# Optimization experiments

Measured on AMD Instinct MI355X. Metric: run time of the kernel, lower is better.

Reference implementation:

```python
import jax, jax.numpy as jnp
import numpy as np

TOP_K = 13
NUM_CLASSES = 80
ALPHA = 1.0
BETA = 6.0
EPS = 1e-9
IOU_EPS = 1e-7


def _ciou(box1, box2, eps=IOU_EPS):
    # box1: gt [B,M,1,4], box2: pred [B,1,A,4], corner format x1y1x2y2
    b1x1, b1y1, b1x2, b1y2 = jnp.split(box1, 4, axis=-1)
    b2x1, b2y1, b2x2, b2y2 = jnp.split(box2, 4, axis=-1)
    w1, h1 = b1x2 - b1x1, b1y2 - b1y1 + eps
    w2, h2 = b2x2 - b2x1, b2y2 - b2y1 + eps
    inter = (jnp.clip(jnp.minimum(b1x2, b2x2) - jnp.maximum(b1x1, b2x1), 0, None)
             * jnp.clip(jnp.minimum(b1y2, b2y2) - jnp.maximum(b1y1, b2y1), 0, None))
    union = w1 * h1 + w2 * h2 - inter + eps
    iou = inter / union
    cw = jnp.maximum(b1x2, b2x2) - jnp.minimum(b1x1, b2x1)  # enclosing box
    ch = jnp.maximum(b1y2, b2y2) - jnp.minimum(b1y1, b2y1)
    c2 = cw ** 2 + ch ** 2 + eps
    rho2 = ((b2x1 + b2x2 - b1x1 - b1x2) ** 2 + (b2y1 + b2y2 - b1y1 - b1y2) ** 2) / 4.0
    v = (4.0 / np.pi ** 2) * (jnp.arctan(w2 / h2) - jnp.arctan(w1 / h1)) ** 2
    alpha = v / (v - iou + (1.0 + eps))
    return (iou - (rho2 / c2 + v * alpha))[..., 0]  # [B,M,A]


def _assign(pred_cls, pred_bbox, anchor_points, gt_cls, gt_bbox, mask_gt):
    B, A, C = pred_cls.shape
    M = gt_bbox.shape[1]
    # --- anchors inside gt boxes: [B,M,A] ---
    lt, rb = gt_bbox[:, :, None, :2], gt_bbox[:, :, None, 2:]   # [B,M,1,2]
    xy = anchor_points[None, None]                               # [1,1,A,2]
    deltas = jnp.concatenate([xy - lt, rb - xy], axis=-1)        # [B,M,A,4]
    mask_in_gts = (deltas.min(-1) > EPS).astype(pred_bbox.dtype)
    mask = mask_in_gts * mask_gt                                 # mask_gt [B,M,1] broadcasts
    # --- box metrics: gather class scores at gt labels, full CIoU grid masked ---
    labels = gt_cls[..., 0].astype(jnp.int32)                    # [B,M]
    idx = jnp.broadcast_to(labels[:, None, :], (B, A, M))
    bbox_scores = jnp.take_along_axis(pred_cls, idx, axis=2).transpose(0, 2, 1) * mask
    overlaps = jnp.clip(_ciou(gt_bbox[:, :, None], pred_bbox[:, None]), 0, None) * mask
    align_metric = bbox_scores ** ALPHA * overlaps ** BETA       # [B,M,A]
    # --- top-k candidate selection (indices of masked-out gts forced to 0, dup counts zeroed) ---
    _, topk_idx = jax.lax.top_k(align_metric, TOP_K)             # [B,M,K]
    topk_mask = jnp.broadcast_to(mask_gt > 0, (B, M, TOP_K))
    topk_idx = jnp.where(topk_mask, topk_idx, 0)
    bi = jnp.arange(B)[:, None, None]
    mi = jnp.arange(M)[None, :, None]
    count = jnp.zeros((B, M, A), jnp.int32).at[bi, mi, topk_idx].add(1)
    mask_topk = jnp.where(count > 1, 0, count).astype(align_metric.dtype)
    mask_pos = mask_topk * mask_in_gts * mask_gt                 # [B,M,A]
    # --- resolve anchors claimed by multiple gts via max overlap ---
    fg = mask_pos.sum(-2)                                        # [B,A]
    is_max = jax.nn.one_hot(overlaps.argmax(1), M, dtype=mask_pos.dtype).transpose(0, 2, 1)
    mask_pos = jnp.where(fg[:, None, :] > 1, is_max, mask_pos)
    fg_mask = mask_pos.sum(-2)                                   # [B,A]
    target_gt_idx = mask_pos.argmax(-2)                          # [B,A]
    # --- gather targets ---
    flat = target_gt_idx + jnp.arange(B)[:, None] * M
    target_labels = labels.reshape(-1)[flat]                     # [B,A]
    target_bbox = gt_bbox.reshape(-1, 4)[flat]                   # [B,A,4]
    target_cls = jnp.where(fg_mask[..., None] > 0,
                           jax.nn.one_hot(target_labels, C, dtype=pred_cls.dtype), 0.0)
    # --- normalize scores by aligned metric ---
    align_metric = align_metric * mask_pos
    pos_align = align_metric.max(-1, keepdims=True)              # [B,M,1]
    pos_overlap = (overlaps * mask_pos).max(-1, keepdims=True)   # [B,M,1]
    norm = (align_metric * pos_overlap / (pos_align + EPS)).max(-2)[..., None]  # [B,A,1]
    target_cls = target_cls * norm
    return target_cls, target_bbox, fg_mask


def setup_inputs() -> dict:
    key = jax.random.key(0)
    ks = jax.random.split(key, 8)
    B, A, C, M = 16, 8400, 80, 32
    anchor_points = jax.random.uniform(ks[0], (A, 2)) * 80.0
    pred_cls = jax.random.uniform(ks[1], (B, A, C))  # sigmoid-like scores in [0,1)
    ctr = anchor_points[None] + jax.random.normal(ks[2], (B, A, 2)) * 2.0
    sz = jax.random.uniform(ks[3], (B, A, 2)) * 15.0 + 2.0
    pred_bbox = jnp.concatenate([ctr - sz / 2, ctr + sz / 2], axis=-1)
    gctr = jax.random.uniform(ks[4], (B, M, 2)) * 80.0
    gsz = jax.random.uniform(ks[5], (B, M, 2)) * 25.0 + 3.0
    gt_bbox = jnp.concatenate([gctr - gsz / 2, gctr + gsz / 2], axis=-1)
    gt_cls = jax.random.randint(ks[6], (B, M, 1), 0, C).astype(jnp.int64)
    mask_gt = (jax.random.uniform(ks[7], (B, M, 1)) < 0.8).astype(jnp.float32)
    return {"pred_cls": pred_cls, "pred_bbox": pred_bbox, "anchor_points": anchor_points,
            "gt_cls": gt_cls, "gt_bbox": gt_bbox, "mask_gt": mask_gt}


def reference(pred_cls, pred_bbox, anchor_points, gt_cls, gt_bbox, mask_gt):
    target_cls, target_bbox, fg_mask = _assign(pred_cls, pred_bbox, anchor_points,
                                               gt_cls, gt_bbox, mask_gt)
    return target_cls, target_bbox, fg_mask.astype(bool)
```

## Files before the change

kernel.cpp:

```cpp
#include <hip/hip_runtime.h>
#include <cstdint>
#include <cstddef>

#define BB 16
#define AA 8400
#define CC 80
#define MM 32
#define TOPK 13
#define NW 8
#define CANCH 1056

__device__ __forceinline__ float ciou_clip(
    float gx1, float gy1, float gx2, float gy2, float at1,
    float4 pb, float w2, float h2, float at2)
{
  const float w1 = gx2 - gx1, h1 = gy2 - gy1 + 1e-7f;
  const float iw = fmaxf(fminf(gx2, pb.z) - fmaxf(gx1, pb.x), 0.f);
  const float ih = fmaxf(fminf(gy2, pb.w) - fmaxf(gy1, pb.y), 0.f);
  const float inter = iw * ih;
  const float uni = w1*h1 + w2*h2 - inter + 1e-7f;
  const float iou = inter / uni;
  const float cw = fmaxf(gx2, pb.z) - fminf(gx1, pb.x);
  const float ch = fmaxf(gy2, pb.w) - fminf(gy1, pb.y);
  const float c2 = cw*cw + ch*ch + 1e-7f;
  const float rx = pb.x + pb.z - gx1 - gx2;
  const float ry = pb.y + pb.w - gy1 - gy2;
  const float rho2 = (rx*rx + ry*ry) * 0.25f;
  const float dv = at2 - at1;
  const float v = 0.4052847345693511f * dv * dv;
  const float alpha = v / (v - iou + (1.f + 1e-7f));
  return fmaxf(iou - (rho2 / c2 + v * alpha), 0.f);
}

__device__ __forceinline__ unsigned long long pack_key(float val, int a) {
  return ((unsigned long long)__float_as_uint(val) << 32)
       | (unsigned long long)(0xFFFFFFFFu - (unsigned)a);
}
__device__ __forceinline__ int key_anchor(unsigned long long k) {
  return (int)(0xFFFFFFFFu - (unsigned)(k & 0xFFFFFFFFull));
}

__global__ __launch_bounds__(512) void k_topk(
    const float* __restrict__ pred_cls, const float* __restrict__ pred_bbox,
    const float* __restrict__ anchors, const int* __restrict__ gt_cls,
    const float* __restrict__ gt_bbox, const float* __restrict__ mask_gt,
    unsigned long long* __restrict__ topkeys)
{
  const int m = blockIdx.x, b = blockIdx.y;
  const int tid = threadIdx.x;
  const int wave = tid >> 6, lane = tid & 63;

  unsigned long long* tk = topkeys + (size_t)(b*MM + m)*TOPK;
  if (mask_gt[b*MM + m] <= 0.f) {
    if (tid < TOPK) tk[tid] = 0ull;
    return;
  }

  __shared__ unsigned short q[NW][CANCH];
  __shared__ unsigned long long s_top[NW][TOPK];

  const float4 gb = reinterpret_cast<const float4*>(gt_bbox)[b*MM + m];
  const float at1 = atanf((gb.z - gb.x) / (gb.w - gb.y + 1e-7f));
  const int lbl = gt_cls[b*MM + m];
  const float*  clsbase = pred_cls + (size_t)b*AA*CC;
  const float4* pbase   = reinterpret_cast<const float4*>(pred_bbox) + (size_t)b*AA;
  const float2* axy     = reinterpret_cast<const float2*>(anchors);

  unsigned long long k13[TOPK];
  #pragma unroll
  for (int i = 0; i < TOPK; ++i) k13[i] = 0ull;

  if (wave == 0) {
    const int a = lane;
    const float2 xy = axy[a];
    const float mind = fminf(fminf(xy.x - gb.x, xy.y - gb.y),
                             fminf(gb.z - xy.x, gb.w - xy.y));
    float val = 0.f;
    if (mind > 1e-9f) {
      const float4 pb = pbase[a];
      const float w2 = pb.z - pb.x, h2 = pb.w - pb.y + 1e-7f;
      const float at2 = atanf(w2 / h2);
      const float ov = ciou_clip(gb.x, gb.y, gb.z, gb.w, at1, pb, w2, h2, at2);
      const float o2 = ov * ov;
      val = clsbase[(size_t)a*CC + lbl] * (o2 * o2 * o2);
    }
    k13[0] = pack_key(val, a);
  }

  const int abase = wave * CANCH;
  int qc = 0;
  for (int s = 0; s < 17; ++s) {
    const int la = s*64 + lane;
    const int a  = abase + la;
    bool pass = false;
    if (la < CANCH && a < AA && !(wave == 0 && a < 64)) {
      const float2 xy = axy[a];
      const float mind = fminf(fminf(xy.x - gb.x, xy.y - gb.y),
                               fminf(gb.z - xy.x, gb.w - xy.y));
      pass = mind > 1e-9f;
    }
    const unsigned long long bal = __ballot(pass);
    if (pass) {
      const int pos = qc + (int)__popcll(bal & ((1ull << lane) - 1ull));
      q[wave][pos] = (unsigned short)la;
    }
    qc += (int)__popcll(bal);
  }

  for (int k = lane; k < qc; k += 64) {
    const int a = abase + (int)q[wave][k];
    const float4 pb = pbase[a];
    const float w2 = pb.z - pb.x, h2 = pb.w - pb.y + 1e-7f;
    const float at2 = atanf(w2 / h2);
    const float ov = ciou_clip(gb.x, gb.y, gb.z, gb.w, at1, pb, w2, h2, at2);
    const float o2 = ov * ov;
    const float val = clsbase[(size_t)a*CC + lbl] * (o2 * o2 * o2);
    const unsigned long long key = pack_key(val, a);
    if (key > k13[TOPK-1]) {
      #pragma unroll
      for (int i = TOPK-1; i >= 1; --i)
        if (key > k13[i]) k13[i] = (key > k13[i-1]) ? k13[i-1] : key;
      if (key > k13[0]) k13[0] = key;
    }
  }

  for (int r = 0; r < TOPK; ++r) {
    unsigned long long bk = k13[0];
    #pragma unroll
    for (int off = 32; off; off >>= 1) {
      const unsigned long long o = __shfl_xor(bk, off);
      if (o > bk) bk = o;
    }
    if (k13[0] == bk) {
      #pragma unroll
      for (int i = 0; i < TOPK-1; ++i) k13[i] = k13[i+1];
      k13[TOPK-1] = 0ull;
    }
    if (lane == 0) s_top[wave][r] = bk;
  }
  __syncthreads();
  if (wave != 0) return;

  unsigned long long v0 = 0ull, v1 = 0ull;
  {
    const int e0 = lane, e1 = lane + 64;
    v0 = s_top[e0/TOPK][e0%TOPK];
    if (e1 < NW*TOPK) v1 = s_top[e1/TOPK][e1%TOPK];
  }
  for (int r = 0; r < TOPK; ++r) {
    const bool s1 = v1 > v0;
    unsigned long long bk = s1 ? v1 : v0;
    const unsigned long long my = bk;
    #pragma unroll
    for (int off = 32; off; off >>= 1) {
      const unsigned long long o = __shfl_xor(bk, off);
      if (o > bk) bk = o;
    }
    if (lane == 0) tk[r] = bk;
    if (my == bk && bk != 0ull) {
      if (s1) v1 = 0ull; else v0 = 0ull;
    }
  }
}

__global__ __launch_bounds__(512) void k_assign(
    const float* __restrict__ pred_cls, const float* __restrict__ pred_bbox,
    const float* __restrict__ anchors, const int* __restrict__ gt_cls,
    const float* __restrict__ gt_bbox, const float* __restrict__ mask_gt,
    const unsigned long long* __restrict__ topkeys,
    float* __restrict__ out_cls, float* __restrict__ out_bbox,
    float* __restrict__ out_fg)
{
  const int b = blockIdx.x / 17, ch = blockIdx.x % 17;
  const int tid = threadIdx.x;
  const int lane = tid & 63;
  const int w0 = ch * 512;
  const int nw = (w0 + 512 <= AA) ? 512 : (AA - w0);

  __shared__ unsigned int s_claim[AA];
  __shared__ unsigned short s_list[MM*TOPK];
  __shared__ int s_ncl;
  __shared__ unsigned char s_asg[512];
  __shared__ float s_av[512];
  __shared__ unsigned int s_pal[MM], s_pov[MM];
  __shared__ float4 s_gb[MM];
  __shared__ float s_at[MM], s_mgt[MM];
  __shared__ int s_lbl[MM];

  const float2* axy   = reinterpret_cast<const float2*>(anchors);
  const float4* pbase = reinterpret_cast<const float4*>(pred_bbox) + (size_t)b*AA;

  if (tid < MM) {
    const float4 g = reinterpret_cast<const float4*>(gt_bbox)[b*MM + tid];
    s_gb[tid] = g;
    s_at[tid] = atanf((g.z - g.x) / (g.w - g.y + 1e-7f));
    s_lbl[tid] = gt_cls[b*MM + tid];
    s_mgt[tid] = mask_gt[b*MM + tid];
    s_pal[tid] = 0u; s_pov[tid] = 0u;
  }
  if (tid == 0) s_ncl = 0;
  s_asg[tid] = 255;
  for (int k = tid; k < AA; k += 512) s_claim[k] = 0u;
  __syncthreads();

  if (tid < MM*TOPK) {
    const int m = tid / TOPK;
    const unsigned long long key = topkeys[(size_t)(b*MM + m)*TOPK + tid%TOPK];
    const int a = key_anchor(key);
    if ((unsigned)a < (unsigned)AA) {
      const float2 xy = axy[a];
      const float4 g = s_gb[m];
      const float mind = fminf(fminf(xy.x - g.x, xy.y - g.y),
                               fminf(g.z - xy.x, g.w - xy.y));
      if (mind > 1e-9f) atomicOr(&s_claim[a], 1u << m);
    }
  }
  __syncthreads();

  for (int a = tid; a < AA; a += 512) {
    const bool c = s_claim[a] != 0u;
    const unsigned long long bal = __ballot(c);
    int base = 0;
    if (lane == 0 && bal) base = atomicAdd(&s_ncl, (int)__popcll(bal));
    base = __shfl(base, 0);
    if (c) s_list[base + (int)__popcll(bal & ((1ull << lane) - 1ull))]
             = (unsigned short)a;
  }
  __syncthreads();
  const int ncl = s_ncl;

  for (int k = tid; k < ncl; k += 512) {
    const int a = (int)s_list[k];
    const unsigned cb = s_claim[a];
    const float4 pb = pbase[a];
    const float2 xy = axy[a];
    const float w2 = pb.z - pb.x, h2 = pb.w - pb.y + 1e-7f;
    const float at2 = atanf(w2 / h2);
    int asg; float bestov;
    if (__popc(cb) == 1) {
      asg = __ffs(cb) - 1;
      const float4 g = s_gb[asg];
      bestov = ciou_clip(g.x, g.y, g.z, g.w, s_at[asg], pb, w2, h2, at2);
    } else {
      float best = -1.f; int bm = 0;
      for (int m = 0; m < MM; ++m) {
        float ov = 0.f;
        const float4 g = s_gb[m];
        const float mind = fminf(fminf(xy.x - g.x, xy.y - g.y),
                                 fminf(g.z - xy.x, g.w - xy.y));
        if (mind > 1e-9f && s_mgt[m] > 0.f)
          ov = ciou_clip(g.x, g.y, g.z, g.w, s_at[m], pb, w2, h2, at2);
        if (ov > best) { best = ov; bm = m; }
      }
      asg = bm; bestov = best;
    }
    const float o2 = bestov * bestov;
    const float av = pred_cls[(size_t)(b*AA + a)*CC + s_lbl[asg]] * (o2*o2*o2);
    atomicMax(&s_pal[asg], __float_as_uint(av));
    atomicMax(&s_pov[asg], __float_as_uint(bestov));
    const int wi = a - w0;
    if ((unsigned)wi < (unsigned)nw) { s_asg[wi] = (unsigned char)asg; s_av[wi] = av; }
  }
  __syncthreads();

  float4* ocw = reinterpret_cast<float4*>(out_cls) + ((size_t)(b*AA + w0)) * (CC/4);
  for (int j = tid; j < nw*(CC/4); j += 512) {
    const int ai = j / (CC/4);
    const int q4 = j % (CC/4);
    const int asg = s_asg[ai];
    float4 o = make_float4(0.f, 0.f, 0.f, 0.f);
    if (asg != 255) {
      const float norm = s_av[ai] * __uint_as_float(s_pov[asg])
                       / (__uint_as_float(s_pal[asg]) + 1e-9f);
      const int lbl = s_lbl[asg];
      const int c0 = q4 * 4;
      if (lbl == c0    ) o.x = norm;
      if (lbl == c0 + 1) o.y = norm;
      if (lbl == c0 + 2) o.z = norm;
      if (lbl == c0 + 3) o.w = norm;
    }
    ocw[j] = o;
  }
  if (tid < nw) {
    const int a = w0 + tid;
    const int asg = s_asg[tid];
    const int tgt = (asg != 255) ? asg : 0;
    reinterpret_cast<float4*>(out_bbox)[b*AA + a] = s_gb[tgt];
    out_fg[b*AA + a] = (asg != 255) ? 1.f : 0.f;
  }
}

extern "C" void kernel_launch(void* const* d_in, const int* in_sizes, int n_in,
                              void* d_out, int out_size, void* d_ws, size_t ws_size,
                              hipStream_t stream)
{
  const float* pred_cls  = (const float*)d_in[0];
  const float* pred_bbox = (const float*)d_in[1];
  const float* anchors   = (const float*)d_in[2];
  const int*   gt_cls    = (const int*)  d_in[3];
  const float* gt_bbox   = (const float*)d_in[4];
  const float* mask_gt   = (const float*)d_in[5];

  unsigned long long* topkeys = (unsigned long long*)d_ws;

  float* out_cls  = (float*)d_out;
  float* out_bbox = out_cls + (size_t)BB*AA*CC;
  float* out_fg   = out_bbox + (size_t)BB*AA*4;

  k_topk<<<dim3(MM, BB), 512, 0, stream>>>(
      pred_cls, pred_bbox, anchors, gt_cls, gt_bbox, mask_gt, topkeys);
  k_assign<<<dim3(BB*17), 512, 0, stream>>>(
      pred_cls, pred_bbox, anchors, gt_cls, gt_bbox, mask_gt, topkeys,
      out_cls, out_bbox, out_fg);
}
```

Before: 48.61 us.

## Split top-k anchor scan across two blocks per GT and merge in assign

Each GT's top-k search is split into two blocks that each cover half of the anchors and write a partial top-13 list. The assign kernel then loads both partial lists into shared memory and merge-selects the final 13 per GT. This doubles the top-k grid from 512 to 1024 blocks to improve GPU occupancy and shorten per-block work. In exchange it adds a serial merge step and a larger workspace for keys.

```diff
diff --git a/kernel.cpp b/kernel.cpp
--- a/kernel.cpp
+++ b/kernel.cpp
@@ -8,7 +8,8 @@
 #define MM 32
 #define TOPK 13
 #define NW 8
-#define CANCH 1056
+#define HANCH 4224
+#define CANCH 528
 
 __device__ __forceinline__ float ciou_clip(
     float gx1, float gy1, float gx2, float gy2, float at1,
@@ -46,11 +47,11 @@
     const float* __restrict__ gt_bbox, const float* __restrict__ mask_gt,
     unsigned long long* __restrict__ topkeys)
 {
-  const int m = blockIdx.x, b = blockIdx.y;
+  const int m = blockIdx.x >> 1, half = blockIdx.x & 1, b = blockIdx.y;
   const int tid = threadIdx.x;
   const int wave = tid >> 6, lane = tid & 63;
 
-  unsigned long long* tk = topkeys + (size_t)(b*MM + m)*TOPK;
+  unsigned long long* tk = topkeys + ((size_t)(b*MM + m)*2 + half)*TOPK;
   if (mask_gt[b*MM + m] <= 0.f) {
     if (tid < TOPK) tk[tid] = 0ull;
     return;
@@ -70,7 +71,7 @@
   #pragma unroll
   for (int i = 0; i < TOPK; ++i) k13[i] = 0ull;
 
-  if (wave == 0) {
+  if (half == 0 && wave == 0) {
     const int a = lane;
     const float2 xy = axy[a];
     const float mind = fminf(fminf(xy.x - gb.x, xy.y - gb.y),
@@ -87,13 +88,13 @@
     k13[0] = pack_key(val, a);
   }
 
-  const int abase = wave * CANCH;
+  const int abase = half*HANCH + wave*CANCH;
   int qc = 0;
-  for (int s = 0; s < 17; ++s) {
+  for (int s = 0; s < 9; ++s) {
     const int la = s*64 + lane;
     const int a  = abase + la;
     bool pass = false;
-    if (la < CANCH && a < AA && !(wave == 0 && a < 64)) {
+    if (la < CANCH && a < AA && !(half == 0 && wave == 0 && la < 64)) {
       const float2 xy = axy[a];
       const float mind = fminf(fminf(xy.x - gb.x, xy.y - gb.y),
                                fminf(gb.z - xy.x, gb.w - xy.y));
@@ -178,6 +179,8 @@
   const int nw = (w0 + 512 <= AA) ? 512 : (AA - w0);
 
   __shared__ unsigned int s_claim[AA];
+  __shared__ unsigned long long s_keys[MM*2*TOPK];
+  __shared__ int s_sel[MM][TOPK];
   __shared__ unsigned short s_list[MM*TOPK];
   __shared__ int s_ncl;
   __shared__ unsigned char s_asg[512];
@@ -200,13 +203,26 @@
   }
   if (tid == 0) s_ncl = 0;
   s_asg[tid] = 255;
+  for (int k = tid; k < MM*2*TOPK; k += 512)
+    s_keys[k] = topkeys[(size_t)b*MM*2*TOPK + k];
   for (int k = tid; k < AA; k += 512) s_claim[k] = 0u;
+  __syncthreads();
+
+  if (tid < MM) {
+    const unsigned long long* A = s_keys + (size_t)tid*2*TOPK;
+    const unsigned long long* B = A + TOPK;
+    int i = 0, j = 0;
+    for (int r = 0; r < TOPK; ++r) {
+      const unsigned long long ka = A[i], kb = B[j];
+      if (ka >= kb) { s_sel[tid][r] = key_anchor(ka); ++i; }
+      else          { s_sel[tid][r] = key_anchor(kb); ++j; }
+    }
+  }
   __syncthreads();
 
   if (tid < MM*TOPK) {
     const int m = tid / TOPK;
-    const unsigned long long key = topkeys[(size_t)(b*MM + m)*TOPK + tid%TOPK];
-    const int a = key_anchor(key);
+    const int a = s_sel[m][tid % TOPK];
     if ((unsigned)a < (unsigned)AA) {
       const float2 xy = axy[a];
       const float4 g = s_gb[m];
@@ -307,7 +323,7 @@
   float* out_bbox = out_cls + (size_t)BB*AA*CC;
   float* out_fg   = out_bbox + (size_t)BB*AA*4;
 
-  k_topk<<<dim3(MM, BB), 512, 0, stream>>>(
+  k_topk<<<dim3(MM*2, BB), 512, 0, stream>>>(
       pred_cls, pred_bbox, anchors, gt_cls, gt_bbox, mask_gt, topkeys);
   k_assign<<<dim3(BB*17), 512, 0, stream>>>(
       pred_cls, pred_bbox, anchors, gt_cls, gt_bbox, mask_gt, topkeys,
```

After: 60.50 us. +24.4%, slower.

## Split assignment into per-batch position kernel and wide output-writing kernel

Applied to the files above, without the earlier changes.

Before, each of the 17 chunk blocks per batch recomputed the full anchor assignment, then wrote only its own window. Now one block per batch computes the claim, assignment and per-gt max statistics once and stores them in workspace. A second kernel with many small 256-thread blocks reads that state back and writes the dense class, bbox and foreground outputs. This removes the redundant recomputation and spreads the large output writes over more blocks, at the cost of an extra launch, a global-memory round trip and only 16 blocks in the compute stage.

```diff
diff --git a/kernel.cpp b/kernel.cpp
--- a/kernel.cpp
+++ b/kernel.cpp
@@ -163,25 +163,21 @@
   }
 }
 
-__global__ __launch_bounds__(512) void k_assign(
+__global__ __launch_bounds__(512) void k_pos(
     const float* __restrict__ pred_cls, const float* __restrict__ pred_bbox,
     const float* __restrict__ anchors, const int* __restrict__ gt_cls,
     const float* __restrict__ gt_bbox, const float* __restrict__ mask_gt,
     const unsigned long long* __restrict__ topkeys,
-    float* __restrict__ out_cls, float* __restrict__ out_bbox,
-    float* __restrict__ out_fg)
-{
-  const int b = blockIdx.x / 17, ch = blockIdx.x % 17;
+    unsigned char* __restrict__ asg_arr, float* __restrict__ av_arr,
+    float* __restrict__ pos_align, float* __restrict__ pos_ovl)
+{
+  const int b = blockIdx.x;
   const int tid = threadIdx.x;
   const int lane = tid & 63;
-  const int w0 = ch * 512;
-  const int nw = (w0 + 512 <= AA) ? 512 : (AA - w0);
 
   __shared__ unsigned int s_claim[AA];
   __shared__ unsigned short s_list[MM*TOPK];
   __shared__ int s_ncl;
-  __shared__ unsigned char s_asg[512];
-  __shared__ float s_av[512];
   __shared__ unsigned int s_pal[MM], s_pov[MM];
   __shared__ float4 s_gb[MM];
   __shared__ float s_at[MM], s_mgt[MM];
@@ -199,8 +195,10 @@
     s_pal[tid] = 0u; s_pov[tid] = 0u;
   }
   if (tid == 0) s_ncl = 0;
-  s_asg[tid] = 255;
-  for (int k = tid; k < AA; k += 512) s_claim[k] = 0u;
+  for (int a = tid; a < AA; a += 512) {
+    s_claim[a] = 0u;
+    asg_arr[(size_t)b*AA + a] = 255;
+  }
   __syncthreads();
 
   if (tid < MM*TOPK) {
@@ -258,20 +256,57 @@
     const float av = pred_cls[(size_t)(b*AA + a)*CC + s_lbl[asg]] * (o2*o2*o2);
     atomicMax(&s_pal[asg], __float_as_uint(av));
     atomicMax(&s_pov[asg], __float_as_uint(bestov));
-    const int wi = a - w0;
-    if ((unsigned)wi < (unsigned)nw) { s_asg[wi] = (unsigned char)asg; s_av[wi] = av; }
-  }
-  __syncthreads();
-
-  float4* ocw = reinterpret_cast<float4*>(out_cls) + ((size_t)(b*AA + w0)) * (CC/4);
-  for (int j = tid; j < nw*(CC/4); j += 512) {
+    asg_arr[(size_t)b*AA + a] = (unsigned char)asg;
+    av_arr[(size_t)b*AA + a]  = av;
+  }
+  __syncthreads();
+
+  if (tid < MM) {
+    pos_align[b*MM + tid] = __uint_as_float(s_pal[tid]);
+    pos_ovl[b*MM + tid]   = __uint_as_float(s_pov[tid]);
+  }
+}
+
+__global__ __launch_bounds__(256) void k_out(
+    const unsigned char* __restrict__ asg_arr, const float* __restrict__ av_arr,
+    const float* __restrict__ pos_align, const float* __restrict__ pos_ovl,
+    const int* __restrict__ gt_cls, const float* __restrict__ gt_bbox,
+    float* __restrict__ out_cls, float* __restrict__ out_bbox,
+    float* __restrict__ out_fg)
+{
+  const int b = blockIdx.x / 66, win = blockIdx.x % 66;
+  const int tid = threadIdx.x;
+  const int a0 = win * 128;
+  const int na = (a0 + 128 <= AA) ? 128 : (AA - a0);
+
+  __shared__ float4 s_gb[MM];
+  __shared__ float s_pal[MM], s_pov[MM];
+  __shared__ int s_lbl[MM];
+  __shared__ unsigned char s_asg[128];
+  __shared__ float s_av[128];
+
+  if (tid < MM) {
+    s_gb[tid]  = reinterpret_cast<const float4*>(gt_bbox)[b*MM + tid];
+    s_lbl[tid] = gt_cls[b*MM + tid];
+    s_pal[tid] = pos_align[b*MM + tid];
+    s_pov[tid] = pos_ovl[b*MM + tid];
+  }
+  if (tid < 128 && tid < na) {
+    const size_t ba = (size_t)b*AA + a0 + tid;
+    const unsigned char g = asg_arr[ba];
+    s_asg[tid] = g;
+    s_av[tid]  = (g != 255) ? av_arr[ba] : 0.f;
+  }
+  __syncthreads();
+
+  float4* ocw = reinterpret_cast<float4*>(out_cls) + ((size_t)(b*AA + a0)) * (CC/4);
+  for (int j = tid; j < na*(CC/4); j += 256) {
     const int ai = j / (CC/4);
     const int q4 = j % (CC/4);
     const int asg = s_asg[ai];
     float4 o = make_float4(0.f, 0.f, 0.f, 0.f);
     if (asg != 255) {
-      const float norm = s_av[ai] * __uint_as_float(s_pov[asg])
-                       / (__uint_as_float(s_pal[asg]) + 1e-9f);
+      const float norm = s_av[ai] * s_pov[asg] / (s_pal[asg] + 1e-9f);
       const int lbl = s_lbl[asg];
       const int c0 = q4 * 4;
       if (lbl == c0    ) o.x = norm;
@@ -281,8 +316,8 @@
     }
     ocw[j] = o;
   }
-  if (tid < nw) {
-    const int a = w0 + tid;
+  if (tid < na) {
+    const int a = a0 + tid;
     const int asg = s_asg[tid];
     const int tgt = (asg != 255) ? asg : 0;
     reinterpret_cast<float4*>(out_bbox)[b*AA + a] = s_gb[tgt];
@@ -301,7 +336,12 @@
   const float* gt_bbox   = (const float*)d_in[4];
   const float* mask_gt   = (const float*)d_in[5];
 
-  unsigned long long* topkeys = (unsigned long long*)d_ws;
+  char* ws = (char*)d_ws;
+  unsigned long long* topkeys = (unsigned long long*)(ws);
+  float* pos_align = (float*)(ws + 53248);
+  float* pos_ovl   = (float*)(ws + 55296);
+  unsigned char* asg_arr = (unsigned char*)(ws + 57344);
+  float* av_arr    = (float*)(ws + 192000);
 
   float* out_cls  = (float*)d_out;
   float* out_bbox = out_cls + (size_t)BB*AA*CC;
@@ -309,7 +349,10 @@
 
   k_topk<<<dim3(MM, BB), 512, 0, stream>>>(
       pred_cls, pred_bbox, anchors, gt_cls, gt_bbox, mask_gt, topkeys);
-  k_assign<<<dim3(BB*17), 512, 0, stream>>>(
+  k_pos<<<dim3(BB), 512, 0, stream>>>(
       pred_cls, pred_bbox, anchors, gt_cls, gt_bbox, mask_gt, topkeys,
+      asg_arr, av_arr, pos_align, pos_ovl);
+  k_out<<<dim3(BB*66), 256, 0, stream>>>(
+      asg_arr, av_arr, pos_align, pos_ovl, gt_cls, gt_bbox,
       out_cls, out_bbox, out_fg);
 }
```

New measurement: 56.10 us. 15.4% more time.
